# Optimization experiments

Measured on AMD Instinct MI355X. Metric: run time of the kernel, lower is better.

Reference implementation:

```python
import jax, jax.numpy as jnp
import numpy as np

REG = 0.1          # entropic regularization, as in the module
N_ITERS = 100      # fixed Sinkhorn iteration count (POT numItermax capped; see notes)


def _sqdist(x, y):
    # ot.dist default: squared Euclidean pairwise distances, [n, m]
    x2 = jnp.sum(x * x, axis=1)[:, None]
    y2 = jnp.sum(y * y, axis=1)[None, :]
    M = x2 + y2 - 2.0 * (x @ y.T)
    return jnp.maximum(M, 0.0)


def setup_inputs() -> dict:
    key = jax.random.key(0)
    kx, ky = jax.random.split(key)
    n, m, d = 4096, 4096, 32
    # uniform in [0, 0.5) keeps exp(-M/reg) representable in fp32
    x = jax.random.uniform(kx, (n, d), dtype=jnp.float32) * 0.5
    y = jax.random.uniform(ky, (m, d), dtype=jnp.float32) * 0.5
    return {"x": x, "y": y}


def reference(x, y):
    n, m = x.shape[0], y.shape[0]
    a = jnp.full((n,), 1.0 / n, dtype=x.dtype)   # uniform source marginal
    b = jnp.full((m,), 1.0 / m, dtype=y.dtype)   # uniform target marginal
    M = _sqdist(x, y)                            # [n, m] cost
    K = jnp.exp(-M / REG)                        # [n, m] Gibbs kernel

    u0 = jnp.full((n,), 1.0 / n, dtype=x.dtype)
    v0 = jnp.full((m,), 1.0 / m, dtype=y.dtype)

    def step(carry, _):
        u, v = carry
        u = a / (K @ v)      # [n]
        v = b / (K.T @ u)    # [m]
        return (u, v), None

    (u, v), _ = jax.lax.scan(step, (u0, v0), None, length=N_ITERS)
    # transport plan gamma = diag(u) K diag(v), as returned by ot.bregman.sinkhorn
    gamma = u[:, None] * K * v[None, :]
    return gamma
```

## Files before the change

### kernel.cpp

```cpp
#include <hip/hip_runtime.h>
#include <hip/hip_fp16.h>


#define NN 4096
#define MM 4096
#define DD 32
#define N_ITERS 100

static constexpr float INV_REG = 10.0f;
static constexpr float A_MARG  = 1.0f / 4096.0f;
static constexpr float B_MARG  = 1.0f / 4096.0f;

typedef _Float16 h2_t __attribute__((ext_vector_type(2)));

static __device__ __forceinline__ float dot2(unsigned a, unsigned b, float acc) {
#if __has_builtin(__builtin_amdgcn_fdot2)
    return __builtin_amdgcn_fdot2(__builtin_bit_cast(h2_t, a),
                                  __builtin_bit_cast(h2_t, b), acc, false);
#else
    float2 fa = __half22float2(*(const __half2*)&a);
    float2 fb = __half22float2(*(const __half2*)&b);
    acc = fmaf(fa.x, fb.x, acc);
    return fmaf(fa.y, fb.y, acc);
#endif
}

static __device__ __forceinline__ unsigned ld_dev_u32(const unsigned* p) {
    return __hip_atomic_load(p, __ATOMIC_RELAXED, __HIP_MEMORY_SCOPE_AGENT);
}
static __device__ __forceinline__ void st_dev_u32(unsigned* p, unsigned v) {
    __hip_atomic_store(p, v, __ATOMIC_RELAXED, __HIP_MEMORY_SCOPE_AGENT);
}
static __device__ __forceinline__ unsigned short ld_dev_u16(const unsigned short* p) {
    return __hip_atomic_load(p, __ATOMIC_RELAXED, __HIP_MEMORY_SCOPE_AGENT);
}
static __device__ __forceinline__ void st_dev_u16(unsigned short* p, unsigned short v) {
    __hip_atomic_store(p, v, __ATOMIC_RELAXED, __HIP_MEMORY_SCOPE_AGENT);
}
static __device__ __forceinline__ unsigned long long ld_dev_u64(const unsigned long long* p) {
    return __hip_atomic_load(p, __ATOMIC_RELAXED, __HIP_MEMORY_SCOPE_AGENT);
}
static __device__ __forceinline__ void st_dev_u64(unsigned long long* p, unsigned long long v) {
    __hip_atomic_store(p, v, __ATOMIC_RELAXED, __HIP_MEMORY_SCOPE_AGENT);
}

__global__ void compute_K_half(const float* __restrict__ p, const float* __restrict__ q,
                               __half* __restrict__ Kh, __half* __restrict__ v16,
                               unsigned* __restrict__ conv, unsigned* __restrict__ slot,
                               unsigned* __restrict__ mtu, unsigned* __restrict__ mtv,
                               int prime) {
    const int tid = threadIdx.x;
    const int j   = blockIdx.x * 256 + tid;
    const int r0  = blockIdx.y * 16;

    if (prime && blockIdx.y == 0) {
        v16[j] = __float2half(B_MARG);
        if (blockIdx.x == 0) {
            if (tid == 0) { *conv = 0u; *slot = 1u; }
            mtu[tid] = 0u; mtu[tid + 256] = 0u;
            mtv[tid] = 0u; mtv[tid + 256] = 0u;
        }
    }

    float qv[DD];
    const float4* q4 = (const float4*)(q + (size_t)j * DD);
#pragma unroll
    for (int k = 0; k < DD / 4; ++k) {
        float4 t = q4[k];
        qv[4 * k + 0] = t.x; qv[4 * k + 1] = t.y;
        qv[4 * k + 2] = t.z; qv[4 * k + 3] = t.w;
    }

    __shared__ float ps[16 * DD];
    ps[tid]       = p[(size_t)r0 * DD + tid];
    ps[tid + 256] = p[(size_t)r0 * DD + tid + 256];
    __syncthreads();

#pragma unroll 4
    for (int ii = 0; ii < 16; ++ii) {
        float acc = 0.0f;
#pragma unroll
        for (int k = 0; k < DD; ++k) {
            float d = ps[ii * DD + k] - qv[k];
            acc = fmaf(d, d, acc);
        }
        Kh[(size_t)(r0 + ii) * MM + j] = __float2half(__expf(-acc * INV_REG));
    }
}

__global__ void __launch_bounds__(1024, 8)
sinkhorn_persist(const __half* __restrict__ Kh, const __half* __restrict__ KTh,
                 float* __restrict__ u32g, float* __restrict__ v32g,
                 unsigned* __restrict__ mtu, unsigned* __restrict__ mtv,
                 unsigned long long* __restrict__ mdu,
                 unsigned long long* __restrict__ mdv) {
    __shared__ __align__(16) __half vlds[MM];
    __shared__ float part[16];
    __shared__ unsigned fb_lds[8];
    const int tid  = threadIdx.x;
    const int lane = tid & 63;
    const int w    = tid >> 6;
    const int rib  = w >> 1;
    const int hlf  = w & 1;
    const int bid  = blockIdx.x;
    const int i    = bid * 8 + rib;
    const int g0   = hlf * 256 + lane;
    const uint4* __restrict__ MU = (const uint4*)(Kh  + (size_t)i * MM);
    const uint4* __restrict__ MV = (const uint4*)(KTh + (size_t)i * MM);

    const uint4 ku0 = MU[g0], ku1 = MU[g0 + 64], ku2 = MU[g0 + 128], ku3 = MU[g0 + 192];
    const uint4 kv0 = MV[g0], kv1 = MV[g0 + 64], kv2 = MV[g0 + 128], kv3 = MV[g0 + 192];

    unsigned long long h0p = ~0ULL, h1p = ~0ULL;

    for (int t = 0; t < N_ITERS; ++t) {
        if (t == 0) {
            if (tid < 512) {
                const unsigned long long dv =
                    (unsigned long long)__half_as_ushort(__float2half(B_MARG)) *
                    0x0001000100010001ULL;
                ((unsigned long long*)vlds)[2 * tid]     = dv;
                ((unsigned long long*)vlds)[2 * tid + 1] = dv;
            }
            __syncthreads();
        } else {
            if (tid < 512) {
                const unsigned want = 2u * (unsigned)t;
                unsigned tg;
                for (;;) {
                    tg = ld_dev_u32(mtv + tid);
                    if ((tg & 0x7fffffffu) == want) break;
                    __builtin_amdgcn_s_sleep(1);
                }
                asm volatile("" ::: "memory");
                unsigned long long d0 = ld_dev_u64(mdv + 2 * tid);
                unsigned long long d1 = ld_dev_u64(mdv + 2 * tid + 1);
                ((unsigned long long*)vlds)[2 * tid]     = d0;
                ((unsigned long long*)vlds)[2 * tid + 1] = d1;
                const bool allf = __all((tg >> 31) != 0u);
                if ((tid & 63) == 0) fb_lds[tid >> 6] = allf ? 1u : 0u;
            }
            __syncthreads();
            if ((t & 1) == 0) {
                if ((fb_lds[0] & fb_lds[1] & fb_lds[2] & fb_lds[3] &
                     fb_lds[4] & fb_lds[5] & fb_lds[6] & fb_lds[7]) != 0u)
                    break;
            }
        }

        {
            const uint4* V = (const uint4*)vlds;
            const uint4 a = V[g0], b = V[g0 + 64], c = V[g0 + 128], d = V[g0 + 192];
            float x0 = 0.f, x1 = 0.f, x2 = 0.f, x3 = 0.f;
            x0 = dot2(ku0.x, a.x, x0); x0 = dot2(ku0.y, a.y, x0);
            x0 = dot2(ku0.z, a.z, x0); x0 = dot2(ku0.w, a.w, x0);
            x1 = dot2(ku1.x, b.x, x1); x1 = dot2(ku1.y, b.y, x1);
            x1 = dot2(ku1.z, b.z, x1); x1 = dot2(ku1.w, b.w, x1);
            x2 = dot2(ku2.x, c.x, x2); x2 = dot2(ku2.y, c.y, x2);
            x2 = dot2(ku2.z, c.z, x2); x2 = dot2(ku2.w, c.w, x2);
            x3 = dot2(ku3.x, d.x, x3); x3 = dot2(ku3.y, d.y, x3);
            x3 = dot2(ku3.z, d.z, x3); x3 = dot2(ku3.w, d.w, x3);
            float acc = (x0 + x1) + (x2 + x3);
#pragma unroll
            for (int off = 32; off > 0; off >>= 1) acc += __shfl_down(acc, off, 64);
            if (lane == 0) part[w] = acc;
        }
        __syncthreads();
        if (w == 0) {
            unsigned hb = 0u;
            if (lane < 8) {
                float r = A_MARG / (part[2 * lane] + part[2 * lane + 1]);
                u32g[bid * 8 + lane] = r;
                hb = (unsigned)__half_as_ushort(__float2half(r));
            }
            const unsigned q0 = __shfl(hb, 0, 64), q1 = __shfl(hb, 1, 64);
            const unsigned q2 = __shfl(hb, 2, 64), q3 = __shfl(hb, 3, 64);
            const unsigned q4 = __shfl(hb, 4, 64), q5 = __shfl(hb, 5, 64);
            const unsigned q6 = __shfl(hb, 6, 64), q7 = __shfl(hb, 7, 64);
            if (lane == 0) {
                const unsigned long long d0 =
                    (unsigned long long)(q0 | (q1 << 16)) |
                    ((unsigned long long)(q2 | (q3 << 16)) << 32);
                const unsigned long long d1 =
                    (unsigned long long)(q4 | (q5 << 16)) |
                    ((unsigned long long)(q6 | (q7 << 16)) << 32);
                st_dev_u64(mdu + 2 * bid,     d0);
                st_dev_u64(mdu + 2 * bid + 1, d1);
                asm volatile("s_waitcnt vmcnt(0)" ::: "memory");
                st_dev_u32(mtu + bid, 2u * (unsigned)t + 1u);
            }
        }

        if (tid < 512) {
            const unsigned want = 2u * (unsigned)t + 1u;
            unsigned tg;
            for (;;) {
                tg = ld_dev_u32(mtu + tid);
                if ((tg & 0x7fffffffu) == want) break;
                __builtin_amdgcn_s_sleep(1);
            }
            asm volatile("" ::: "memory");
            unsigned long long d0 = ld_dev_u64(mdu + 2 * tid);
            unsigned long long d1 = ld_dev_u64(mdu + 2 * tid + 1);
            ((unsigned long long*)vlds)[2 * tid]     = d0;
            ((unsigned long long*)vlds)[2 * tid + 1] = d1;
        }
        __syncthreads();

        {
            const uint4* V = (const uint4*)vlds;
            const uint4 a = V[g0], b = V[g0 + 64], c = V[g0 + 128], d = V[g0 + 192];
            float x0 = 0.f, x1 = 0.f, x2 = 0.f, x3 = 0.f;
            x0 = dot2(kv0.x, a.x, x0); x0 = dot2(kv0.y, a.y, x0);
            x0 = dot2(kv0.z, a.z, x0); x0 = dot2(kv0.w, a.w, x0);
            x1 = dot2(kv1.x, b.x, x1); x1 = dot2(kv1.y, b.y, x1);
            x1 = dot2(kv1.z, b.z, x1); x1 = dot2(kv1.w, b.w, x1);
            x2 = dot2(kv2.x, c.x, x2); x2 = dot2(kv2.y, c.y, x2);
            x2 = dot2(kv2.z, c.z, x2); x2 = dot2(kv2.w, c.w, x2);
            x3 = dot2(kv3.x, d.x, x3); x3 = dot2(kv3.y, d.y, x3);
            x3 = dot2(kv3.z, d.z, x3); x3 = dot2(kv3.w, d.w, x3);
            float acc = (x0 + x1) + (x2 + x3);
#pragma unroll
            for (int off = 32; off > 0; off >>= 1) acc += __shfl_down(acc, off, 64);
            if (lane == 0) part[w] = acc;
        }
        __syncthreads();
        if (w == 0) {
            unsigned hb = 0u;
            if (lane < 8) {
                float r = B_MARG / (part[2 * lane] + part[2 * lane + 1]);
                v32g[bid * 8 + lane] = r;
                hb = (unsigned)__half_as_ushort(__float2half(r));
            }
            const unsigned q0 = __shfl(hb, 0, 64), q1 = __shfl(hb, 1, 64);
            const unsigned q2 = __shfl(hb, 2, 64), q3 = __shfl(hb, 3, 64);
            const unsigned q4 = __shfl(hb, 4, 64), q5 = __shfl(hb, 5, 64);
            const unsigned q6 = __shfl(hb, 6, 64), q7 = __shfl(hb, 7, 64);
            if (lane == 0) {
                const unsigned long long d0 =
                    (unsigned long long)(q0 | (q1 << 16)) |
                    ((unsigned long long)(q2 | (q3 << 16)) << 32);
                const unsigned long long d1 =
                    (unsigned long long)(q4 | (q5 << 16)) |
                    ((unsigned long long)(q6 | (q7 << 16)) << 32);
                unsigned tg = 2u * (unsigned)t + 2u;
                if (t & 1) {
                    if (d0 == h0p && d1 == h1p) tg |= 0x80000000u;
                    h0p = d0; h1p = d1;
                }
                st_dev_u64(mdv + 2 * bid,     d0);
                st_dev_u64(mdv + 2 * bid + 1, d1);
                asm volatile("s_waitcnt vmcnt(0)" ::: "memory");
                st_dev_u32(mtv + bid, tg);
            }
        }
    }
}

__global__ void __launch_bounds__(1024, 8)
rowpass_u(const __half* __restrict__ Mat, const __half* __restrict__ w16_in,
          float* __restrict__ w32_out, __half* __restrict__ w16_out,
          unsigned* __restrict__ conv, unsigned* __restrict__ slot, int t) {
    if (ld_dev_u32(conv)) return;
    if ((t & 1) == 0) {
        if (ld_dev_u32(slot) == 0u) {
            if (threadIdx.x == 0) st_dev_u32(conv, 1u);
            return;
        }
    } else {
        if (blockIdx.x == 0 && threadIdx.x == 0) st_dev_u32(slot, 0u);
    }

    __shared__ __align__(16) __half vlds[MM];
    __shared__ float part[16];
    const int tid  = threadIdx.x;
    const int lane = tid & 63;
    const int w    = tid >> 6;
    const int rib  = w >> 1;
    const int hlf  = w & 1;
    const int i    = blockIdx.x * 8 + rib;
    const uint4* __restrict__ Mrow = (const uint4*)(Mat + (size_t)i * MM);
    const int g0 = hlf * 256 + lane;

    uint4 stg;
    if (tid < 512) stg = ((const uint4*)w16_in)[tid];
    const uint4 k0 = Mrow[g0];
    const uint4 k1 = Mrow[g0 + 64];
    const uint4 k2 = Mrow[g0 + 128];
    const uint4 k3 = Mrow[g0 + 192];
    if (tid < 512) ((uint4*)vlds)[tid] = stg;
    __syncthreads();

    const uint4* V = (const uint4*)vlds;
    const uint4 v0 = V[g0];
    const uint4 v1 = V[g0 + 64];
    const uint4 v2 = V[g0 + 128];
    const uint4 v3 = V[g0 + 192];

    float a0 = 0.f, a1 = 0.f, a2 = 0.f, a3 = 0.f;
    a0 = dot2(k0.x, v0.x, a0); a0 = dot2(k0.y, v0.y, a0);
    a0 = dot2(k0.z, v0.z, a0); a0 = dot2(k0.w, v0.w, a0);
    a1 = dot2(k1.x, v1.x, a1); a1 = dot2(k1.y, v1.y, a1);
    a1 = dot2(k1.z, v1.z, a1); a1 = dot2(k1.w, v1.w, a1);
    a2 = dot2(k2.x, v2.x, a2); a2 = dot2(k2.y, v2.y, a2);
    a2 = dot2(k2.z, v2.z, a2); a2 = dot2(k2.w, v2.w, a2);
    a3 = dot2(k3.x, v3.x, a3); a3 = dot2(k3.y, v3.y, a3);
    a3 = dot2(k3.z, v3.z, a3); a3 = dot2(k3.w, v3.w, a3);
    float acc = (a0 + a1) + (a2 + a3);

#pragma unroll
    for (int off = 32; off > 0; off >>= 1) acc += __shfl_down(acc, off, 64);
    if (lane == 0) part[w] = acc;
    __syncthreads();

    if (tid < 8) {
        const int row = blockIdx.x * 8 + tid;
        float r = A_MARG / (part[2 * tid] + part[2 * tid + 1]);
        w32_out[row] = r;
        w16_out[row] = __float2half(r);
    }
}

__global__ void __launch_bounds__(1024, 8)
rowpass_v(const __half* __restrict__ Mat, const __half* __restrict__ w16_in,
          float* __restrict__ w32_out, __half* __restrict__ w16_out,
          unsigned short* __restrict__ hist,
          unsigned* __restrict__ conv, unsigned* __restrict__ slot, int t) {
    if (ld_dev_u32(conv)) return;

    __shared__ __align__(16) __half vlds[MM];
    __shared__ float part[16];
    const int tid  = threadIdx.x;
    const int lane = tid & 63;
    const int w    = tid >> 6;
    const int rib  = w >> 1;
    const int hlf  = w & 1;
    const int i    = blockIdx.x * 8 + rib;
    const uint4* __restrict__ Mrow = (const uint4*)(Mat + (size_t)i * MM);
    const int g0 = hlf * 256 + lane;

    uint4 stg;
    if (tid < 512) stg = ((const uint4*)w16_in)[tid];
    const uint4 k0 = Mrow[g0];
    const uint4 k1 = Mrow[g0 + 64];
    const uint4 k2 = Mrow[g0 + 128];
    const uint4 k3 = Mrow[g0 + 192];
    if (tid < 512) ((uint4*)vlds)[tid] = stg;
    __syncthreads();

    const uint4* V = (const uint4*)vlds;
    const uint4 v0 = V[g0];
    const uint4 v1 = V[g0 + 64];
    const uint4 v2 = V[g0 + 128];
    const uint4 v3 = V[g0 + 192];

    float a0 = 0.f, a1 = 0.f, a2 = 0.f, a3 = 0.f;
    a0 = dot2(k0.x, v0.x, a0); a0 = dot2(k0.y, v0.y, a0);
    a0 = dot2(k0.z, v0.z, a0); a0 = dot2(k0.w, v0.w, a0);
    a1 = dot2(k1.x, v1.x, a1); a1 = dot2(k1.y, v1.y, a1);
    a1 = dot2(k1.z, v1.z, a1); a1 = dot2(k1.w, v1.w, a1);
    a2 = dot2(k2.x, v2.x, a2); a2 = dot2(k2.y, v2.y, a2);
    a2 = dot2(k2.z, v2.z, a2); a2 = dot2(k2.w, v2.w, a2);
    a3 = dot2(k3.x, v3.x, a3); a3 = dot2(k3.y, v3.y, a3);
    a3 = dot2(k3.z, v3.z, a3); a3 = dot2(k3.w, v3.w, a3);
    float acc = (a0 + a1) + (a2 + a3);

#pragma unroll
    for (int off = 32; off > 0; off >>= 1) acc += __shfl_down(acc, off, 64);
    if (lane == 0) part[w] = acc;
    __syncthreads();

    if (tid < 8) {
        const int row = blockIdx.x * 8 + tid;
        float r = B_MARG / (part[2 * tid] + part[2 * tid + 1]);
        w32_out[row] = r;
        const __half h = __float2half(r);
        if (t & 1) {
            const unsigned short bits = __half_as_ushort(h);
            const unsigned short old2 = ld_dev_u16(hist + row);
            if (old2 != bits) st_dev_u32(slot, 1u);
            st_dev_u16(hist + row, bits);
        }
        w16_out[row] = h;
    }
}

__global__ void epilogue(const float* __restrict__ x, const float* __restrict__ y,
                         const float* __restrict__ u, const float* __restrict__ v,
                         float* __restrict__ out) {
    const int tid = threadIdx.x;
    const int j   = blockIdx.x * 256 + tid;
    const int r0  = blockIdx.y * 16;

    float yv[DD];
    const float4* y4 = (const float4*)(y + (size_t)j * DD);
#pragma unroll
    for (int k = 0; k < DD / 4; ++k) {
        float4 t = y4[k];
        yv[4 * k + 0] = t.x; yv[4 * k + 1] = t.y;
        yv[4 * k + 2] = t.z; yv[4 * k + 3] = t.w;
    }

    __shared__ float xs[16 * DD];
    __shared__ float u_lds[16];
    xs[tid]       = x[(size_t)r0 * DD + tid];
    xs[tid + 256] = x[(size_t)r0 * DD + tid + 256];
    if (tid < 16) u_lds[tid] = u[r0 + tid];
    __syncthreads();

    const float vj = v[j];
#pragma unroll 4
    for (int ii = 0; ii < 16; ++ii) {
        float acc = 0.0f;
#pragma unroll
        for (int k = 0; k < DD; ++k) {
            float d = xs[ii * DD + k] - yv[k];
            acc = fmaf(d, d, acc);
        }
        out[(size_t)(r0 + ii) * MM + j] = u_lds[ii] * __expf(-acc * INV_REG) * vj;
    }
}

extern "C" void kernel_launch(void* const* d_in, const int* in_sizes, int n_in,
                              void* d_out, int out_size, void* d_ws, size_t ws_size,
                              hipStream_t stream) {
    const float* x = (const float*)d_in[0];
    const float* y = (const float*)d_in[1];
    __half*   Kh   = (__half*)d_ws;
    __half*   KTh  = Kh + (size_t)NN * MM;
    float*    u32  = (float*)(KTh + (size_t)NN * MM);
    float*    v32  = u32 + NN;
    __half*   u16  = (__half*)(v32 + MM);
    __half*   v16  = u16 + NN;
    unsigned short* hist = (unsigned short*)(v16 + MM);
    unsigned* slot = (unsigned*)(hist + MM);
    unsigned* conv = slot + 1;
    unsigned* mtu  = slot + 512;
    unsigned* mtv  = mtu + 512;
    unsigned long long* mdu = (unsigned long long*)(mtv + 512);
    unsigned long long* mdv = mdu + 1024;
    float*    out  = (float*)d_out;

    compute_K_half<<<dim3(MM / 256, NN / 16), 256, 0, stream>>>(x, y, Kh, v16, conv, slot, mtu, mtv, 1);
    compute_K_half<<<dim3(NN / 256, MM / 16), 256, 0, stream>>>(y, x, KTh, v16, conv, slot, mtu, mtv, 0);

    {
        void* args[] = { &Kh, &KTh, &u32, &v32, &mtu, &mtv, &mdu, &mdv };
        hipError_t e = hipLaunchCooperativeKernel((const void*)sinkhorn_persist,
                                                  dim3(512), dim3(1024), args, 0, stream);
        if (e != hipSuccess) {
            (void)hipGetLastError();
            for (int t = 0; t < N_ITERS; ++t) {
                rowpass_u<<<NN / 8, 1024, 0, stream>>>(Kh,  v16, u32, u16, conv, slot, t);
                rowpass_v<<<MM / 8, 1024, 0, stream>>>(KTh, u16, v32, v16, hist, conv, slot, t);
            }
        }
    }

    epilogue<<<dim3(MM / 256, NN / 16), 256, 0, stream>>>(x, y, u32, v32, out);
}
```

Baseline: 614.5 us.

## Pack each fp16 value with its phase tag into one word for exchange

Swaps the per-block flag plus separate 64-bit data mailbox for per-element 32-bit words. Each word carries the fp16 value in its high half and an iteration tag with a convergence bit in its low half. Producers write straight from 8 lanes with no shuffles, no waitcnt and no ordering between data and flag. Consumers poll 8 words per thread and re-poll only the stale ones. This drops a serialized store-then-flag round trip per half-iteration, at the cost of more polling loads per thread.

```diff
diff --git a/kernel.cpp b/kernel.cpp
--- a/kernel.cpp
+++ b/kernel.cpp
@@ -37,17 +37,11 @@
 static __device__ __forceinline__ void st_dev_u16(unsigned short* p, unsigned short v) {
     __hip_atomic_store(p, v, __ATOMIC_RELAXED, __HIP_MEMORY_SCOPE_AGENT);
 }
-static __device__ __forceinline__ unsigned long long ld_dev_u64(const unsigned long long* p) {
-    return __hip_atomic_load(p, __ATOMIC_RELAXED, __HIP_MEMORY_SCOPE_AGENT);
-}
-static __device__ __forceinline__ void st_dev_u64(unsigned long long* p, unsigned long long v) {
-    __hip_atomic_store(p, v, __ATOMIC_RELAXED, __HIP_MEMORY_SCOPE_AGENT);
-}
 
 __global__ void compute_K_half(const float* __restrict__ p, const float* __restrict__ q,
                                __half* __restrict__ Kh, __half* __restrict__ v16,
                                unsigned* __restrict__ conv, unsigned* __restrict__ slot,
-                               unsigned* __restrict__ mtu, unsigned* __restrict__ mtv,
+                               unsigned* __restrict__ mbu, unsigned* __restrict__ mbv,
                                int prime) {
     const int tid = threadIdx.x;
     const int j   = blockIdx.x * 256 + tid;
@@ -55,11 +49,9 @@
 
     if (prime && blockIdx.y == 0) {
         v16[j] = __float2half(B_MARG);
-        if (blockIdx.x == 0) {
-            if (tid == 0) { *conv = 0u; *slot = 1u; }
-            mtu[tid] = 0u; mtu[tid + 256] = 0u;
-            mtv[tid] = 0u; mtv[tid + 256] = 0u;
-        }
+        mbu[j] = 0u;
+        mbv[j] = 0u;
+        if (blockIdx.x == 0 && tid == 0) { *conv = 0u; *slot = 1u; }
     }
 
     float qv[DD];
@@ -91,9 +83,7 @@
 __global__ void __launch_bounds__(1024, 8)
 sinkhorn_persist(const __half* __restrict__ Kh, const __half* __restrict__ KTh,
                  float* __restrict__ u32g, float* __restrict__ v32g,
-                 unsigned* __restrict__ mtu, unsigned* __restrict__ mtv,
-                 unsigned long long* __restrict__ mdu,
-                 unsigned long long* __restrict__ mdv) {
+                 unsigned* __restrict__ mbu, unsigned* __restrict__ mbv) {
     __shared__ __align__(16) __half vlds[MM];
     __shared__ float part[16];
     __shared__ unsigned fb_lds[8];
@@ -107,11 +97,12 @@
     const int g0   = hlf * 256 + lane;
     const uint4* __restrict__ MU = (const uint4*)(Kh  + (size_t)i * MM);
     const uint4* __restrict__ MV = (const uint4*)(KTh + (size_t)i * MM);
+    unsigned short* __restrict__ vlh = (unsigned short*)vlds;
 
     const uint4 ku0 = MU[g0], ku1 = MU[g0 + 64], ku2 = MU[g0 + 128], ku3 = MU[g0 + 192];
     const uint4 kv0 = MV[g0], kv1 = MV[g0 + 64], kv2 = MV[g0 + 128], kv3 = MV[g0 + 192];
 
-    unsigned long long h0p = ~0ULL, h1p = ~0ULL;
+    unsigned histv = 0x10000u;
 
     for (int t = 0; t < N_ITERS; ++t) {
         if (t == 0) {
@@ -125,19 +116,28 @@
             __syncthreads();
         } else {
             if (tid < 512) {
-                const unsigned want = 2u * (unsigned)t;
-                unsigned tg;
+                const unsigned want = (unsigned)(2 * t) & 0x7fffu;
+                unsigned g[8];
+#pragma unroll
+                for (int k = 0; k < 8; ++k) g[k] = ld_dev_u32(mbv + (k << 9) + tid);
                 for (;;) {
-                    tg = ld_dev_u32(mtv + tid);
-                    if ((tg & 0x7fffffffu) == want) break;
+                    unsigned bad = 0u;
+#pragma unroll
+                    for (int k = 0; k < 8; ++k)
+                        if ((g[k] & 0x7fffu) != want) bad |= 1u << k;
+                    if (!bad) break;
                     __builtin_amdgcn_s_sleep(1);
+#pragma unroll
+                    for (int k = 0; k < 8; ++k)
+                        if (bad & (1u << k)) g[k] = ld_dev_u32(mbv + (k << 9) + tid);
                 }
-                asm volatile("" ::: "memory");
-                unsigned long long d0 = ld_dev_u64(mdv + 2 * tid);
-                unsigned long long d1 = ld_dev_u64(mdv + 2 * tid + 1);
-                ((unsigned long long*)vlds)[2 * tid]     = d0;
-                ((unsigned long long*)vlds)[2 * tid + 1] = d1;
-                const bool allf = __all((tg >> 31) != 0u);
+                unsigned fzb = 0x8000u;
+#pragma unroll
+                for (int k = 0; k < 8; ++k) {
+                    vlh[(k << 9) + tid] = (unsigned short)(g[k] >> 16);
+                    fzb &= g[k];
+                }
+                const bool allf = __all(fzb != 0u);
                 if ((tid & 63) == 0) fb_lds[tid >> 6] = allf ? 1u : 0u;
             }
             __syncthreads();
@@ -166,44 +166,33 @@
             if (lane == 0) part[w] = acc;
         }
         __syncthreads();
-        if (w == 0) {
-            unsigned hb = 0u;
-            if (lane < 8) {
-                float r = A_MARG / (part[2 * lane] + part[2 * lane + 1]);
-                u32g[bid * 8 + lane] = r;
-                hb = (unsigned)__half_as_ushort(__float2half(r));
-            }
-            const unsigned q0 = __shfl(hb, 0, 64), q1 = __shfl(hb, 1, 64);
-            const unsigned q2 = __shfl(hb, 2, 64), q3 = __shfl(hb, 3, 64);
-            const unsigned q4 = __shfl(hb, 4, 64), q5 = __shfl(hb, 5, 64);
-            const unsigned q6 = __shfl(hb, 6, 64), q7 = __shfl(hb, 7, 64);
-            if (lane == 0) {
-                const unsigned long long d0 =
-                    (unsigned long long)(q0 | (q1 << 16)) |
-                    ((unsigned long long)(q2 | (q3 << 16)) << 32);
-                const unsigned long long d1 =
-                    (unsigned long long)(q4 | (q5 << 16)) |
-                    ((unsigned long long)(q6 | (q7 << 16)) << 32);
-                st_dev_u64(mdu + 2 * bid,     d0);
-                st_dev_u64(mdu + 2 * bid + 1, d1);
-                asm volatile("s_waitcnt vmcnt(0)" ::: "memory");
-                st_dev_u32(mtu + bid, 2u * (unsigned)t + 1u);
-            }
+        if (tid < 8) {
+            float r = A_MARG / (part[2 * tid] + part[2 * tid + 1]);
+            u32g[bid * 8 + tid] = r;
+            const unsigned val = (unsigned)__half_as_ushort(__float2half(r));
+            st_dev_u32(mbu + bid * 8 + tid,
+                       (val << 16) | ((unsigned)(2 * t + 1) & 0x7fffu));
         }
 
         if (tid < 512) {
-            const unsigned want = 2u * (unsigned)t + 1u;
-            unsigned tg;
+            const unsigned want = (unsigned)(2 * t + 1) & 0x7fffu;
+            unsigned g[8];
+#pragma unroll
+            for (int k = 0; k < 8; ++k) g[k] = ld_dev_u32(mbu + (k << 9) + tid);
             for (;;) {
-                tg = ld_dev_u32(mtu + tid);
-                if ((tg & 0x7fffffffu) == want) break;
+                unsigned bad = 0u;
+#pragma unroll
+                for (int k = 0; k < 8; ++k)
+                    if ((g[k] & 0x7fffu) != want) bad |= 1u << k;
+                if (!bad) break;
                 __builtin_amdgcn_s_sleep(1);
-            }
-            asm volatile("" ::: "memory");
-            unsigned long long d0 = ld_dev_u64(mdu + 2 * tid);
-            unsigned long long d1 = ld_dev_u64(mdu + 2 * tid + 1);
-            ((unsigned long long*)vlds)[2 * tid]     = d0;
-            ((unsigned long long*)vlds)[2 * tid + 1] = d1;
+#pragma unroll
+                for (int k = 0; k < 8; ++k)
+                    if (bad & (1u << k)) g[k] = ld_dev_u32(mbu + (k << 9) + tid);
+            }
+#pragma unroll
+            for (int k = 0; k < 8; ++k)
+                vlh[(k << 9) + tid] = (unsigned short)(g[k] >> 16);
         }
         __syncthreads();
 
@@ -225,34 +214,16 @@
             if (lane == 0) part[w] = acc;
         }
         __syncthreads();
-        if (w == 0) {
-            unsigned hb = 0u;
-            if (lane < 8) {
-                float r = B_MARG / (part[2 * lane] + part[2 * lane + 1]);
-                v32g[bid * 8 + lane] = r;
-                hb = (unsigned)__half_as_ushort(__float2half(r));
-            }
-            const unsigned q0 = __shfl(hb, 0, 64), q1 = __shfl(hb, 1, 64);
-            const unsigned q2 = __shfl(hb, 2, 64), q3 = __shfl(hb, 3, 64);
-            const unsigned q4 = __shfl(hb, 4, 64), q5 = __shfl(hb, 5, 64);
-            const unsigned q6 = __shfl(hb, 6, 64), q7 = __shfl(hb, 7, 64);
-            if (lane == 0) {
-                const unsigned long long d0 =
-                    (unsigned long long)(q0 | (q1 << 16)) |
-                    ((unsigned long long)(q2 | (q3 << 16)) << 32);
-                const unsigned long long d1 =
-                    (unsigned long long)(q4 | (q5 << 16)) |
-                    ((unsigned long long)(q6 | (q7 << 16)) << 32);
-                unsigned tg = 2u * (unsigned)t + 2u;
-                if (t & 1) {
-                    if (d0 == h0p && d1 == h1p) tg |= 0x80000000u;
-                    h0p = d0; h1p = d1;
-                }
-                st_dev_u64(mdv + 2 * bid,     d0);
-                st_dev_u64(mdv + 2 * bid + 1, d1);
-                asm volatile("s_waitcnt vmcnt(0)" ::: "memory");
-                st_dev_u32(mtv + bid, tg);
-            }
+        if (tid < 8) {
+            float r = B_MARG / (part[2 * tid] + part[2 * tid + 1]);
+            v32g[bid * 8 + tid] = r;
+            const unsigned val = (unsigned)__half_as_ushort(__float2half(r));
+            unsigned ph = (unsigned)(2 * t + 2) & 0x7fffu;
+            if (t & 1) {
+                if (val == histv) ph |= 0x8000u;
+                histv = val;
+            }
+            st_dev_u32(mbv + bid * 8 + tid, (val << 16) | ph);
         }
     }
 }
@@ -435,17 +406,15 @@
     unsigned short* hist = (unsigned short*)(v16 + MM);
     unsigned* slot = (unsigned*)(hist + MM);
     unsigned* conv = slot + 1;
-    unsigned* mtu  = slot + 512;
-    unsigned* mtv  = mtu + 512;
-    unsigned long long* mdu = (unsigned long long*)(mtv + 512);
-    unsigned long long* mdv = mdu + 1024;
+    unsigned* mbu  = slot + 512;
+    unsigned* mbv  = mbu + NN;
     float*    out  = (float*)d_out;
 
-    compute_K_half<<<dim3(MM / 256, NN / 16), 256, 0, stream>>>(x, y, Kh, v16, conv, slot, mtu, mtv, 1);
-    compute_K_half<<<dim3(NN / 256, MM / 16), 256, 0, stream>>>(y, x, KTh, v16, conv, slot, mtu, mtv, 0);
+    compute_K_half<<<dim3(MM / 256, NN / 16), 256, 0, stream>>>(x, y, Kh, v16, conv, slot, mbu, mbv, 1);
+    compute_K_half<<<dim3(NN / 256, MM / 16), 256, 0, stream>>>(y, x, KTh, v16, conv, slot, mbu, mbv, 0);
 
     {
-        void* args[] = { &Kh, &KTh, &u32, &v32, &mtu, &mtv, &mdu, &mdv };
+        void* args[] = { &Kh, &KTh, &u32, &v32, &mbu, &mbv };
         hipError_t e = hipLaunchCooperativeKernel((const void*)sinkhorn_persist,
                                                   dim3(512), dim3(1024), args, 0, stream);
         if (e != hipSuccess) {
```

Result: faster. 576.7 us (-6.2%).
